# Optimization experiments

Measured on AMD Instinct MI355X. Metric: run time of the kernel, lower is better.

## Reference

```python
import jax, jax.numpy as jnp
import numpy as np

B, L, C = 4, 4096, 512
G = 4            # n_groups
H = 16           # n_heads
K = 5            # offset conv kernel == offset_range_factor
GC = C // G      # n_group_channels = 128
HC = C // H      # n_head_channels = 32


def conv1d(x, w, b, pad):
    # x: [N, Cin, L], w: [Cout, Cin, K]
    out = jax.lax.conv_general_dilated(
        x, w, window_strides=(1,), padding=[(pad, pad)],
        dimension_numbers=('NCH', 'OIH', 'NCH'))
    return out + b[None, :, None]


def grid_sample_1d(feats, gy):
    # feats: [Bg, d, L]  gy: [Bg, N] normalized coords in [-1, 1]
    # bilinear, zeros padding, align_corners=False (matches F.grid_sample)
    Bg, d, Lf = feats.shape
    N = gy.shape[-1]
    iy = ((gy + 1.0) * Lf - 1.0) * 0.5
    i0 = jnp.floor(iy)
    w1 = iy - i0
    i0 = i0.astype(jnp.int32)

    def gather(idx):
        valid = ((idx >= 0) & (idx < Lf)).astype(feats.dtype)
        idxc = jnp.clip(idx, 0, Lf - 1)
        g = jnp.take_along_axis(
            feats, jnp.broadcast_to(idxc[:, None, :], (Bg, d, N)), axis=2)
        return g * valid[:, None, :]

    return gather(i0) * (1.0 - w1)[:, None, :] + gather(i0 + 1) * w1[:, None, :]


def setup_inputs() -> dict:
    key = jax.random.key(0)
    ks = jax.random.split(key, 16)
    s = 0.02
    return {
        'x':     jax.random.normal(ks[0], (B, L, C), jnp.float32),
        'Wq':    jax.random.normal(ks[1], (C, C), jnp.float32) * s,
        'bq':    jnp.zeros((C,), jnp.float32),
        'Wk':    jax.random.normal(ks[2], (C, C), jnp.float32) * s,
        'bk':    jnp.zeros((C,), jnp.float32),
        'Wv':    jax.random.normal(ks[3], (C, C), jnp.float32) * s,
        'bv':    jnp.zeros((C,), jnp.float32),
        'Woff1': jax.random.normal(ks[4], (GC, GC, K), jnp.float32) * s,
        'boff1': jnp.zeros((GC,), jnp.float32),
        'Woff2': jax.random.normal(ks[5], (1, GC, 1), jnp.float32) * s,
        'boff2': jnp.zeros((1,), jnp.float32),
        'rpb':   jax.random.normal(ks[6], (1, C, L), jnp.float32) * s,
        'Wout':  jax.random.normal(ks[7], (C, C), jnp.float32) * s,
        'bout':  jnp.zeros((C,), jnp.float32),
    }


def reference(x, Wq, bq, Wk, bk, Wv, bv, Woff1, boff1, Woff2, boff2, rpb, Wout, bout):
    Bx, Lx, Cx = x.shape
    xc = x.transpose(0, 2, 1)                                # [B, C, L]
    # 1x1 conv projections == channel matmuls
    q = jnp.einsum('oc,bcl->bol', Wq, xc) + bq[None, :, None]
    # group queries: 'b (g d) n -> (b g) d n'
    qg = q.reshape(Bx * G, GC, Lx)
    # offset prediction: conv(k=5,pad=2) then conv(k=1,pad=2) -> length L+4
    off = conv1d(qg, Woff1, boff1, pad=K // 2)               # [Bg, GC, L]
    off = conv1d(off, Woff2, boff2, pad=K // 2)[:, 0, :]     # [Bg, L+4]
    off = jnp.tanh(off) * float(K)                           # offset_range_factor
    N = off.shape[-1]
    vgrid = jnp.arange(N, dtype=x.dtype) + off               # [Bg, L+4]
    gy = 2.0 * vgrid / float(max(N - 1, 1)) - 1.0
    # bilinear gather of grouped x, then crop to L
    xg = xc.reshape(Bx * G, GC, Lx)
    xs = grid_sample_1d(xg, gy)[:, :, :Lx]                   # [Bg, GC, L]
    xs = xs.reshape(Bx, Cx, Lx)                              # '(b g) d n -> b (g d) n'
    k = jnp.einsum('oc,bcl->bol', Wk, xs) + bk[None, :, None]
    v = jnp.einsum('oc,bcl->bol', Wv, xs) + bv[None, :, None] + rpb
    # heads: [B*H, HC, L]; attention over the CHANNEL dim (i,j = head channels)
    qh = q.reshape(Bx * H, HC, Lx)
    kh = k.reshape(Bx * H, HC, Lx)
    vh = v.reshape(Bx * H, HC, Lx)
    logits = jnp.einsum('bil,bjl->bij', qh, kh) * (Cx ** -0.5)  # [BH, HC, HC]
    attn = jax.nn.softmax(logits, axis=-1)
    o = jnp.einsum('bij,bjl->bil', attn, vh)                 # [BH, HC, L]
    # '(b g) l c -> b c (g l)' with g=H, l=HC, c=L  ->  [B, L, C]
    o = o.reshape(Bx, H, HC, Lx).transpose(0, 3, 1, 2).reshape(Bx, Lx, Cx)
    return o @ Wout.T + bout
```

## Files before the change

### kernel.cpp

```cpp
#include <hip/hip_runtime.h>
#include <math.h>

#define BB   4
#define LL   4096
#define CC   512
#define GG   4
#define HH   16
#define KW   5
#define GCC  128
#define HCC  32
#define BGN  (BB*GG)
#define BHN  (BB*HH)
#define KSPLIT 16

typedef __attribute__((ext_vector_type(8))) __bf16 bf16x8;
typedef __attribute__((ext_vector_type(4))) float f32x4;

__device__ __forceinline__ unsigned int f2bf_bits(float f) {
    unsigned int u = __float_as_uint(f);
    return (u + 0x7FFFu + ((u >> 16) & 1u)) >> 16;
}
__device__ __forceinline__ float bfbits2f(unsigned int s) {
    return __uint_as_float(s << 16);
}
__device__ __forceinline__ void split2(float v, unsigned short& h, unsigned short& l) {
    unsigned int hb = f2bf_bits(v);
    float hf = bfbits2f(hb);
    unsigned int lb = f2bf_bits(v - hf);
    h = (unsigned short)hb; l = (unsigned short)lb;
}

__device__ __forceinline__ void gload16(const void* g, void* l) {
    __builtin_amdgcn_global_load_lds(
        (const __attribute__((address_space(1))) void*)g,
        (__attribute__((address_space(3))) void*)l, 16, 0, 0);
}

__global__ __launch_bounds__(256) void split_x_kernel(
    const float* __restrict__ in, unsigned short* __restrict__ hi,
    unsigned short* __restrict__ lo, int n4)
{
    int i = blockIdx.x * 256 + threadIdx.x;
    if (i >= n4) return;
    float4 v = ((const float4*)in)[i];
    ushort4 h, l;
    split2(v.x, h.x, l.x); split2(v.y, h.y, l.y);
    split2(v.z, h.z, l.z); split2(v.w, h.w, l.w);
    ((ushort4*)hi)[i] = h;
    ((ushort4*)lo)[i] = l;
}

__global__ __launch_bounds__(256) void split_w_kernel(
    const float* __restrict__ W0, const float* __restrict__ W1,
    const float* __restrict__ W2, const float* __restrict__ W3,
    unsigned short* __restrict__ hi, unsigned short* __restrict__ lo)
{
    int w = blockIdx.y;
    const float* W = (w == 0) ? W0 : (w == 1) ? W1 : (w == 2) ? W2 : W3;
    size_t seg4 = (size_t)w * 65536;
    int i = blockIdx.x * 256 + threadIdx.x;
    float4 v = ((const float4*)W)[i];
    ushort4 h, l;
    split2(v.x, h.x, l.x); split2(v.y, h.y, l.y);
    split2(v.z, h.z, l.z); split2(v.w, h.w, l.w);
    ((ushort4*)hi)[seg4 + i] = h;
    ((ushort4*)lo)[seg4 + i] = l;
}

__global__ __launch_bounds__(256) void gemm_split_mfma(
    const unsigned short* __restrict__ Ahi, const unsigned short* __restrict__ Alo,
    const unsigned short* __restrict__ Bhi, const unsigned short* __restrict__ Blo,
    const float* __restrict__ bias, const float* __restrict__ rpb,
    float* __restrict__ out, int RA, int RB, int Kd,
    size_t aStride, size_t bStride, int biasOnCol)
{
    __shared__ unsigned short sAh[4096];
    __shared__ unsigned short sAl[4096];
    __shared__ unsigned short sBh[4096];
    __shared__ unsigned short sBl[4096];

    const int b  = blockIdx.z;
    const int c0 = blockIdx.x * 128;
    const int r0 = blockIdx.y * 128;

    const int tid  = threadIdx.x;
    const int lane = tid & 63;
    const int wv   = tid >> 6;
    const int wr   = wv >> 1, wc = wv & 1;

    const size_t laneA = (size_t)(r0 + wv * 32 + (lane >> 2)) * Kd + (size_t)((lane & 3) * 8);
    const size_t laneB = (size_t)(c0 + wv * 32 + (lane >> 2)) * Kd + (size_t)((lane & 3) * 8);
    const unsigned short* gAh = Ahi + (size_t)b * aStride + laneA;
    const unsigned short* gAl = Alo + (size_t)b * aStride + laneA;
    const unsigned short* gBh = Bhi + (size_t)b * bStride + laneB;
    const unsigned short* gBl = Blo + (size_t)b * bStride + laneB;
    const size_t rowskip = (size_t)16 * Kd;

    unsigned short* lAh = &sAh[(wv * 32) * 32];
    unsigned short* lAl = &sAl[(wv * 32) * 32];
    unsigned short* lBh = &sBh[(wv * 32) * 32];
    unsigned short* lBl = &sBl[(wv * 32) * 32];

    const int lr = lane & 15, lk = (lane >> 4) * 8;
    const unsigned short* fAh = &sAh[(wr * 64 + lr) * 32 + lk];
    const unsigned short* fAl = &sAl[(wr * 64 + lr) * 32 + lk];
    const unsigned short* fBh = &sBh[(wc * 64 + lr) * 32 + lk];
    const unsigned short* fBl = &sBl[(wc * 64 + lr) * 32 + lk];

    f32x4 acc[4][4];
#pragma unroll
    for (int i = 0; i < 4; ++i)
#pragma unroll
        for (int j = 0; j < 4; ++j) acc[i][j] = (f32x4){0.f, 0.f, 0.f, 0.f};

    for (int k0 = 0; k0 < Kd; k0 += 32) {
        gload16(gAh + k0,           lAh);
        gload16(gAh + k0 + rowskip, lAh + 512);
        gload16(gAl + k0,           lAl);
        gload16(gAl + k0 + rowskip, lAl + 512);
        gload16(gBh + k0,           lBh);
        gload16(gBh + k0 + rowskip, lBh + 512);
        gload16(gBl + k0,           lBl);
        gload16(gBl + k0 + rowskip, lBl + 512);
        __syncthreads();

        bf16x8 ah[4], al[4], bh[4], bl[4];
#pragma unroll
        for (int i = 0; i < 4; ++i) {
            ah[i] = *(const bf16x8*)(fAh + i * 512);
            al[i] = *(const bf16x8*)(fAl + i * 512);
        }
#pragma unroll
        for (int j = 0; j < 4; ++j) {
            bh[j] = *(const bf16x8*)(fBh + j * 512);
            bl[j] = *(const bf16x8*)(fBl + j * 512);
        }
#pragma unroll
        for (int i = 0; i < 4; ++i)
#pragma unroll
            for (int j = 0; j < 4; ++j) {
                acc[i][j] = __builtin_amdgcn_mfma_f32_16x16x32_bf16(ah[i], bh[j], acc[i][j], 0, 0, 0);
                acc[i][j] = __builtin_amdgcn_mfma_f32_16x16x32_bf16(al[i], bh[j], acc[i][j], 0, 0, 0);
                acc[i][j] = __builtin_amdgcn_mfma_f32_16x16x32_bf16(ah[i], bl[j], acc[i][j], 0, 0, 0);
            }
        __syncthreads();
    }

    const int lg4 = (lane >> 4) * 4;
    float bcol[4];
#pragma unroll
    for (int fj = 0; fj < 4; ++fj)
        bcol[fj] = biasOnCol ? bias[c0 + wc * 64 + fj * 16 + lr] : 0.f;

#pragma unroll
    for (int fi = 0; fi < 4; ++fi) {
#pragma unroll
        for (int reg = 0; reg < 4; ++reg) {
            const int r = r0 + wr * 64 + fi * 16 + lg4 + reg;
            const float br = biasOnCol ? 0.f : bias[r];
            float* orow = out + ((size_t)b * RA + r) * RB + c0;
            const float* prow = rpb ? (rpb + (size_t)r * RB + c0) : nullptr;
#pragma unroll
            for (int fj = 0; fj < 4; ++fj) {
                const int c = wc * 64 + fj * 16 + lr;
                float val = acc[fi][fj][reg] + br + bcol[fj];
                if (prow) val += prow[c];
                orow[c] = val;
            }
        }
    }
}

__global__ void comb_weights(const float* __restrict__ Woff1, const float* __restrict__ boff1,
                             const float* __restrict__ Woff2, const float* __restrict__ boff2,
                             float* __restrict__ wc)
{
    int idx = blockIdx.x * 256 + threadIdx.x;
    if (idx < GCC * KW) {
        int cp = idx / KW, t = idx - cp * KW;
        float s = 0.f;
        for (int c = 0; c < GCC; ++c)
            s = fmaf(Woff2[c], Woff1[((size_t)c * GCC + cp) * KW + t], s);
        wc[idx] = s;
    } else if (idx == GCC * KW) {
        float s = boff2[0];
        for (int c = 0; c < GCC; ++c) s = fmaf(Woff2[c], boff1[c], s);
        wc[idx] = s;
    } else if (idx == GCC * KW + 1) {
        wc[idx] = boff2[0];
    }
}

__global__ __launch_bounds__(256) void offsets_kernel(
    const float* __restrict__ q, const float* __restrict__ wc,
    float* __restrict__ offv)
{
    __shared__ float w[GCC * KW + 2];
    for (int i = threadIdx.x; i < GCC * KW + 2; i += 256) w[i] = wc[i];
    __syncthreads();

    int bg = blockIdx.y;
    int l  = blockIdx.x * 256 + threadIdx.x;
    const float* qb = q + (size_t)bg * GCC * LL;

    float acc;
    if (l < 2) {
        acc = w[GCC * KW + 1];
    } else {
        acc = w[GCC * KW];
        if (l >= 4) {
            for (int cp = 0; cp < GCC; ++cp) {
                const float* qr = qb + (size_t)cp * LL + l - 4;
#pragma unroll
                for (int t = 0; t < KW; ++t)
                    acc = fmaf(w[cp * KW + t], qr[t], acc);
            }
        } else {
            for (int cp = 0; cp < GCC; ++cp) {
#pragma unroll
                for (int t = 0; t < KW; ++t) {
                    int ll2 = l + t - 4;
                    if (ll2 >= 0)
                        acc = fmaf(w[cp * KW + t], qb[(size_t)cp * LL + ll2], acc);
                }
            }
        }
    }
    float off = tanhf(acc) * (float)KW;
    float vg  = (float)l + off;
    float iy  = vg * ((float)LL / (float)(LL + 2 * (KW / 2) - 1)) - 0.5f;
    offv[(size_t)bg * LL + l] = iy;
}

__global__ __launch_bounds__(256) void gather_kernel(
    const float* __restrict__ x, const float* __restrict__ offv,
    unsigned short* __restrict__ xshi, unsigned short* __restrict__ xslo)
{
    int bg = blockIdx.y;
    int b = bg >> 2, g = bg & 3;
    int l  = blockIdx.x * 8 + (threadIdx.x >> 5);
    int d4 = (threadIdx.x & 31) * 4;

    float iy = offv[(size_t)bg * LL + l];
    float fi = floorf(iy);
    float w1 = iy - fi;
    int i0 = (int)fi;
    int i1 = i0 + 1;

    const float* xb = x + (size_t)b * LL * CC + (size_t)g * GCC + d4;
    float4 v0 = make_float4(0.f, 0.f, 0.f, 0.f);
    float4 v1 = make_float4(0.f, 0.f, 0.f, 0.f);
    if (i0 >= 0 && i0 < LL) v0 = *(const float4*)(xb + (size_t)i0 * CC);
    if (i1 >= 0 && i1 < LL) v1 = *(const float4*)(xb + (size_t)i1 * CC);
    float w0 = 1.f - w1;
    float4 r = make_float4(v0.x * w0 + v1.x * w1, v0.y * w0 + v1.y * w1,
                           v0.z * w0 + v1.z * w1, v0.w * w0 + v1.w * w1);
    size_t o = ((size_t)b * LL + l) * CC + (size_t)g * GCC + d4;
    ushort4 h, lo4;
    split2(r.x, h.x, lo4.x); split2(r.y, h.y, lo4.y);
    split2(r.z, h.z, lo4.z); split2(r.w, h.w, lo4.w);
    *(ushort4*)(xshi + o) = h;
    *(ushort4*)(xslo + o) = lo4;
}

__global__ __launch_bounds__(64) void qk_logits(
    const float* __restrict__ q, const float* __restrict__ k,
    float* __restrict__ part)
{
    int ks = blockIdx.x, bh = blockIdx.y;
    int b = bh >> 4, h = bh & 15;
    int lane = threadIdx.x;
    int ti = lane >> 3, tj = lane & 7;
    const float* qb = q + ((size_t)b * CC + h * HCC + ti * 4) * LL;
    const float* kb = k + ((size_t)b * CC + h * HCC + tj * 4) * LL;

    float acc[4][4];
#pragma unroll
    for (int i = 0; i < 4; ++i)
#pragma unroll
        for (int j = 0; j < 4; ++j) acc[i][j] = 0.f;

    const int chunk = LL / KSPLIT;
    int l0 = ks * chunk;
    for (int l = l0; l < l0 + chunk; l += 8) {
        float4 qa[4][2], kv[4][2];
#pragma unroll
        for (int p = 0; p < 4; ++p) {
            qa[p][0] = *(const float4*)(qb + (size_t)p * LL + l);
            qa[p][1] = *(const float4*)(qb + (size_t)p * LL + l + 4);
            kv[p][0] = *(const float4*)(kb + (size_t)p * LL + l);
            kv[p][1] = *(const float4*)(kb + (size_t)p * LL + l + 4);
        }
#pragma unroll
        for (int i = 0; i < 4; ++i)
#pragma unroll
            for (int j = 0; j < 4; ++j) {
                float s = acc[i][j];
                s = fmaf(qa[i][0].x, kv[j][0].x, s);
                s = fmaf(qa[i][0].y, kv[j][0].y, s);
                s = fmaf(qa[i][0].z, kv[j][0].z, s);
                s = fmaf(qa[i][0].w, kv[j][0].w, s);
                s = fmaf(qa[i][1].x, kv[j][1].x, s);
                s = fmaf(qa[i][1].y, kv[j][1].y, s);
                s = fmaf(qa[i][1].z, kv[j][1].z, s);
                s = fmaf(qa[i][1].w, kv[j][1].w, s);
                acc[i][j] = s;
            }
    }
#pragma unroll
    for (int i = 0; i < 4; ++i)
#pragma unroll
        for (int j = 0; j < 4; ++j)
            part[(((size_t)bh * KSPLIT + ks) * HCC + ti * 4 + i) * HCC + tj * 4 + j] = acc[i][j];
}

__global__ __launch_bounds__(64) void softmax_kernel(
    const float* __restrict__ part, float* __restrict__ attn)
{
    int bh = blockIdx.x;
    int i = threadIdx.x;
    if (i >= HCC) return;
    const float SCALE = 0.044194173824159216f;

    float lg[HCC];
    float mx = -1e30f;
#pragma unroll
    for (int j = 0; j < HCC; ++j) {
        float s = 0.f;
        for (int ks = 0; ks < KSPLIT; ++ks)
            s += part[(((size_t)bh * KSPLIT + ks) * HCC + i) * HCC + j];
        s *= SCALE;
        lg[j] = s;
        mx = fmaxf(mx, s);
    }
    float sum = 0.f;
#pragma unroll
    for (int j = 0; j < HCC; ++j) {
        float e = expf(lg[j] - mx);
        lg[j] = e;
        sum += e;
    }
    float inv = 1.f / sum;
#pragma unroll
    for (int j = 0; j < HCC; ++j)
        attn[((size_t)bh * HCC + i) * HCC + j] = lg[j] * inv;
}

__global__ __launch_bounds__(256) void attn_v_kernel(
    const float* __restrict__ attn, const float* __restrict__ v,
    unsigned short* __restrict__ ohi, unsigned short* __restrict__ olo)
{
    int bh = blockIdx.y;
    int b = bh >> 4, h = bh & 15;
    int tid = threadIdx.x;
    int i = tid >> 3, lsub = tid & 7;

    float arow[HCC];
#pragma unroll
    for (int j = 0; j < HCC; ++j)
        arow[j] = attn[((size_t)bh * HCC + i) * HCC + j];

    const float* vb = v + ((size_t)b * CC + h * HCC) * LL;
    __shared__ float os[HCC][65];

    for (int l0 = blockIdx.x * 512; l0 < blockIdx.x * 512 + 512; l0 += 64) {
        int lbase = l0 + lsub * 8;
        float4 a0 = make_float4(0.f, 0.f, 0.f, 0.f);
        float4 a1 = make_float4(0.f, 0.f, 0.f, 0.f);
#pragma unroll 8
        for (int j = 0; j < HCC; ++j) {
            float aw = arow[j];
            float4 v0 = *(const float4*)(vb + (size_t)j * LL + lbase);
            float4 v1 = *(const float4*)(vb + (size_t)j * LL + lbase + 4);
            a0.x = fmaf(aw, v0.x, a0.x); a0.y = fmaf(aw, v0.y, a0.y);
            a0.z = fmaf(aw, v0.z, a0.z); a0.w = fmaf(aw, v0.w, a0.w);
            a1.x = fmaf(aw, v1.x, a1.x); a1.y = fmaf(aw, v1.y, a1.y);
            a1.z = fmaf(aw, v1.z, a1.z); a1.w = fmaf(aw, v1.w, a1.w);
        }
        os[i][lsub*8+0] = a0.x; os[i][lsub*8+1] = a0.y;
        os[i][lsub*8+2] = a0.z; os[i][lsub*8+3] = a0.w;
        os[i][lsub*8+4] = a1.x; os[i][lsub*8+5] = a1.y;
        os[i][lsub*8+6] = a1.z; os[i][lsub*8+7] = a1.w;
        __syncthreads();
        int i2 = tid & 31, lw = tid >> 5;
#pragma unroll
        for (int c = 0; c < 8; ++c) {
            int ll = lw * 8 + c;
            float val = os[i2][ll];
            unsigned short hbits, lbits;
            split2(val, hbits, lbits);
            size_t oidx = ((size_t)b * LL + l0 + ll) * CC + h * HCC + i2;
            ohi[oidx] = hbits;
            olo[oidx] = lbits;
        }
        __syncthreads();
    }
}

extern "C" void kernel_launch(void* const* d_in, const int* in_sizes, int n_in,
                              void* d_out, int out_size, void* d_ws, size_t ws_size,
                              hipStream_t stream)
{
    (void)in_sizes; (void)n_in; (void)out_size; (void)ws_size;
    const float* x     = (const float*)d_in[0];
    const float* Wq    = (const float*)d_in[1];
    const float* bq    = (const float*)d_in[2];
    const float* Wk    = (const float*)d_in[3];
    const float* bk    = (const float*)d_in[4];
    const float* Wv    = (const float*)d_in[5];
    const float* bv    = (const float*)d_in[6];
    const float* Woff1 = (const float*)d_in[7];
    const float* boff1 = (const float*)d_in[8];
    const float* Woff2 = (const float*)d_in[9];
    const float* boff2 = (const float*)d_in[10];
    const float* rpb   = (const float*)d_in[11];
    const float* Wout  = (const float*)d_in[12];
    const float* bout  = (const float*)d_in[13];
    float* out = (float*)d_out;

    float* ws = (float*)d_ws;
    float* q    = ws;
    float* kbuf = ws + 8388608;
    float* vbuf = ws + 16777216;
    unsigned short* dhi = (unsigned short*)(ws + 25165824);
    unsigned short* dlo = (unsigned short*)(ws + 25165824 + 4194304);
    unsigned short* whi = (unsigned short*)(ws + 33554432);
    unsigned short* wlo = (unsigned short*)(ws + 33554432 + 524288);
    float* offv = ws + 34603008;
    float* wcmb = ws + 34668544;
    float* part = ws + 34669568;
    float* attn = ws + 35718144;

    const size_t NK = (size_t)LL * CC;

    comb_weights<<<dim3(3), dim3(256), 0, stream>>>(Woff1, boff1, Woff2, boff2, wcmb);
    split_w_kernel<<<dim3(256, 4), dim3(256), 0, stream>>>(Wq, Wk, Wv, Wout, whi, wlo);
    split_x_kernel<<<dim3(8192), dim3(256), 0, stream>>>(x, dhi, dlo, 2097152);

    gemm_split_mfma<<<dim3(32, 4, 4), dim3(256), 0, stream>>>(
        whi + 0 * 262144, wlo + 0 * 262144, dhi, dlo, bq, nullptr,
        q, CC, LL, CC, 0, NK, 0);

    offsets_kernel<<<dim3(16, 16), dim3(256), 0, stream>>>(q, wcmb, offv);
    gather_kernel<<<dim3(512, 16), dim3(256), 0, stream>>>(x, offv, dhi, dlo);

    gemm_split_mfma<<<dim3(32, 4, 4), dim3(256), 0, stream>>>(
        whi + 1 * 262144, wlo + 1 * 262144, dhi, dlo, bk, nullptr,
        kbuf, CC, LL, CC, 0, NK, 0);
    gemm_split_mfma<<<dim3(32, 4, 4), dim3(256), 0, stream>>>(
        whi + 2 * 262144, wlo + 2 * 262144, dhi, dlo, bv, rpb,
        vbuf, CC, LL, CC, 0, NK, 0);

    qk_logits<<<dim3(KSPLIT, BHN), dim3(64), 0, stream>>>(q, kbuf, part);
    softmax_kernel<<<dim3(BHN), dim3(64), 0, stream>>>(part, attn);
    attn_v_kernel<<<dim3(8, BHN), dim3(256), 0, stream>>>(attn, vbuf, dhi, dlo);

    gemm_split_mfma<<<dim3(4, 32, 4), dim3(256), 0, stream>>>(
        dhi, dlo, whi + 3 * 262144, wlo + 3 * 262144, bout, nullptr,
        out, LL, CC, CC, NK, 0, 1);
}
```

Measured before the change: 465.6 us.

## Split offset conv over channel groups with shared-memory tiling and a reduce kernel

The offset convolution kernel is replaced by a two-stage scheme. The first stage tiles q rows into shared memory per 128-position block and splits the 128 input channels into 4 groups across the grid. The second stage sums the partials and applies tanh and the coordinate transform. The old kernel launched only 256 blocks with long serial channel loops; the new one exposes more parallelism and reuses loaded q across the 5 taps. The cost is an extra launch and a partial buffer round trip, which reuses the 'part' workspace later used by qk_logits.

```diff
diff --git a/kernel.cpp b/kernel.cpp
--- a/kernel.cpp
+++ b/kernel.cpp
@@ -191,40 +191,68 @@
     }
 }
 
-__global__ __launch_bounds__(256) void offsets_kernel(
+#define OLT 128
+__global__ __launch_bounds__(128) void offsets_part_kernel(
     const float* __restrict__ q, const float* __restrict__ wc,
+    float* __restrict__ part)
+{
+    __shared__ float sq[32][140];
+    __shared__ float sw[32 * KW];
+
+    const int l0 = blockIdx.x * OLT;
+    const int bg = blockIdx.y;
+    const int cg = blockIdx.z;
+    const int tid = threadIdx.x;
+
+    const float* qb = q + ((size_t)bg * GCC + cg * 32) * LL;
+
+    for (int i = tid; i < 32 * KW; i += 128) sw[i] = wc[cg * 32 * KW + i];
+
+    {
+        const int row = tid >> 2;
+        const int l4  = tid & 3;
+        const float* qrow = qb + (size_t)row * LL + l0 - 8;
+        for (int j = l4; j < 34; j += 4) {
+            int idx = j * 4;
+            float4 v;
+            if (l0 - 8 + idx >= 0) v = *(const float4*)(qrow + idx);
+            else v = make_float4(0.f, 0.f, 0.f, 0.f);
+            *(float4*)&sq[row][idx] = v;
+        }
+    }
+    __syncthreads();
+
+    const int li = tid;
+    float acc = 0.f;
+#pragma unroll
+    for (int cp = 0; cp < 32; ++cp) {
+        const float* r  = &sq[cp][li + 4];
+        const float* wr = &sw[cp * KW];
+        acc = fmaf(wr[0], r[0], acc);
+        acc = fmaf(wr[1], r[1], acc);
+        acc = fmaf(wr[2], r[2], acc);
+        acc = fmaf(wr[3], r[3], acc);
+        acc = fmaf(wr[4], r[4], acc);
+    }
+    part[((size_t)cg * BGN + bg) * LL + l0 + li] = acc;
+}
+
+__global__ __launch_bounds__(256) void offsets_finish_kernel(
+    const float* __restrict__ part, const float* __restrict__ wc,
     float* __restrict__ offv)
 {
-    __shared__ float w[GCC * KW + 2];
-    for (int i = threadIdx.x; i < GCC * KW + 2; i += 256) w[i] = wc[i];
-    __syncthreads();
-
-    int bg = blockIdx.y;
-    int l  = blockIdx.x * 256 + threadIdx.x;
-    const float* qb = q + (size_t)bg * GCC * LL;
-
+    int i = blockIdx.x * 256 + threadIdx.x;
+    int bg = i >> 12;
+    int l  = i & (LL - 1);
     float acc;
     if (l < 2) {
-        acc = w[GCC * KW + 1];
+        acc = wc[GCC * KW + 1];
     } else {
-        acc = w[GCC * KW];
-        if (l >= 4) {
-            for (int cp = 0; cp < GCC; ++cp) {
-                const float* qr = qb + (size_t)cp * LL + l - 4;
-#pragma unroll
-                for (int t = 0; t < KW; ++t)
-                    acc = fmaf(w[cp * KW + t], qr[t], acc);
-            }
-        } else {
-            for (int cp = 0; cp < GCC; ++cp) {
-#pragma unroll
-                for (int t = 0; t < KW; ++t) {
-                    int ll2 = l + t - 4;
-                    if (ll2 >= 0)
-                        acc = fmaf(w[cp * KW + t], qb[(size_t)cp * LL + ll2], acc);
-                }
-            }
-        }
+        acc = wc[GCC * KW]
+            + part[((size_t)0 * BGN + bg) * LL + l]
+            + part[((size_t)1 * BGN + bg) * LL + l]
+            + part[((size_t)2 * BGN + bg) * LL + l]
+            + part[((size_t)3 * BGN + bg) * LL + l];
     }
     float off = tanhf(acc) * (float)KW;
     float vg  = (float)l + off;
@@ -441,7 +469,8 @@
         whi + 0 * 262144, wlo + 0 * 262144, dhi, dlo, bq, nullptr,
         q, CC, LL, CC, 0, NK, 0);
 
-    offsets_kernel<<<dim3(16, 16), dim3(256), 0, stream>>>(q, wcmb, offv);
+    offsets_part_kernel<<<dim3(32, 16, 4), dim3(128), 0, stream>>>(q, wcmb, part);
+    offsets_finish_kernel<<<dim3(256), dim3(256), 0, stream>>>(part, wcmb, offv);
     gather_kernel<<<dim3(512, 16), dim3(256), 0, stream>>>(x, offv, dhi, dlo);
 
     gemm_split_mfma<<<dim3(32, 4, 4), dim3(256), 0, stream>>>(
```

Measured after the change: 401.5 us. 1.16x faster.
